# Kernel optimization log

Hardware: AMD Instinct MI355X
Metric: run time of the kernel (lower is better)

Reference implementation:

```python
import jax, jax.numpy as jnp
import numpy as np

EMB = 1024
HID = 4096
NHEADS = 16
DK = EMB // NHEADS
EPS = 1e-6
B, S = 2, 2048


def setup_inputs() -> dict:
    key = jax.random.key(0)
    ks = jax.random.split(key, 10)
    sc = 0.02
    return {
        "x": jax.random.normal(ks[0], (B, S, EMB), dtype=jnp.float32),
        "src_mask": jnp.ones((B, 1, 1, S), dtype=jnp.int32),
        "wq": jax.random.normal(ks[1], (EMB, EMB), dtype=jnp.float32) * sc,
        "wk": jax.random.normal(ks[2], (EMB, EMB), dtype=jnp.float32) * sc,
        "wv": jax.random.normal(ks[3], (EMB, EMB), dtype=jnp.float32) * sc,
        "wo": jax.random.normal(ks[4], (EMB, EMB), dtype=jnp.float32) * sc,
        "ff1_w": jax.random.normal(ks[5], (EMB, HID), dtype=jnp.float32) * sc,
        "ff1_b": jnp.zeros((HID,), dtype=jnp.float32),
        "ff2_w": jax.random.normal(ks[6], (HID, EMB), dtype=jnp.float32) * sc,
        "ff2_b": jnp.zeros((EMB,), dtype=jnp.float32),
        "ln1_a": jnp.ones((1,), dtype=jnp.float32),
        "ln1_b": jnp.zeros((1,), dtype=jnp.float32),
        "ln2_a": jnp.ones((1,), dtype=jnp.float32),
        "ln2_b": jnp.zeros((1,), dtype=jnp.float32),
    }


def layernorm(x, alpha, bias):
    # Faithful to the custom LayerNorm: scalar alpha/bias, std with Bessel
    # correction (torch default unbiased=True), divide by (std + eps).
    mean = jnp.mean(x, axis=-1, keepdims=True)
    var = jnp.sum((x - mean) ** 2, axis=-1, keepdims=True) / (x.shape[-1] - 1)
    std = jnp.sqrt(var)
    return alpha * (x - mean) / (std + EPS) + bias


def mha(x, mask, wq, wk, wv, wo):
    b, s, _ = x.shape
    def split_heads(t):  # [B,S,E] -> [B,H,S,dk]
        return t.reshape(b, s, NHEADS, DK).transpose(0, 2, 1, 3)
    q = split_heads(x @ wq)
    k = split_heads(x @ wk)
    v = split_heads(x @ wv)
    scores = jnp.einsum("bhqd,bhkd->bhqk", q, k) / jnp.sqrt(jnp.float32(DK))
    scores = jnp.where(mask == 0, -jnp.inf, scores)
    attn = jax.nn.softmax(scores, axis=-1)
    out = jnp.einsum("bhqk,bhkd->bhqd", attn, v)
    out = out.transpose(0, 2, 1, 3).reshape(b, s, EMB)
    return out @ wo


def ffn(x, w1, b1, w2, b2):
    return jax.nn.relu(x @ w1 + b1) @ w2 + b2


def reference(x, src_mask, wq, wk, wv, wo, ff1_w, ff1_b, ff2_w, ff2_b,
              ln1_a, ln1_b, ln2_a, ln2_b):
    # pre-norm residual encoder block (dropout=0 / eval mode)
    h = x + mha(layernorm(x, ln1_a, ln1_b), src_mask, wq, wk, wv, wo)
    out = h + ffn(layernorm(h, ln2_a, ln2_b), ff1_w, ff1_b, ff2_w, ff2_b)
    return out
```

## Files before the change

kernel.cpp:

```cpp
#include <hip/hip_runtime.h>
#include <stdint.h>

#define EMB 1024
#define HID 4096
#define NHEADS 16
#define DKH 64
#define SEQ 2048
#define BATCH 2
#define MROWS (BATCH * SEQ)
#define GBK 64

typedef unsigned short u16;
typedef unsigned int u32;
typedef __attribute__((ext_vector_type(8))) short short8;
typedef __attribute__((ext_vector_type(4))) float f32x4;
typedef __attribute__((ext_vector_type(16))) float f32x16;
typedef __attribute__((ext_vector_type(4))) u32 u32x4;
typedef __attribute__((ext_vector_type(2))) int i32x2;

#if __has_builtin(__builtin_amdgcn_exp2f)
#define QK_SCALE 0.18033688011f
#define QK_CLAMP 43.3f
__device__ __forceinline__ float pexp(float x) { return __builtin_amdgcn_exp2f(x); }
#else
#define QK_SCALE 0.125f
#define QK_CLAMP 30.0f
__device__ __forceinline__ float pexp(float x) { return __expf(x); }
#endif

__device__ __forceinline__ u16 f2bf(float f) {
    unsigned u = __float_as_uint(f);
    unsigned r = 0x7FFFu + ((u >> 16) & 1u);
    return (u16)((u + r) >> 16);
}
__device__ __forceinline__ f32x4 mfma16(short8 a, short8 b, f32x4 c) {
    return __builtin_amdgcn_mfma_f32_16x16x32_bf16(a, b, c, 0, 0, 0);
}
__device__ __forceinline__ f32x16 mfma32(short8 a, short8 b, f32x16 c) {
    return __builtin_amdgcn_mfma_f32_32x32x16_bf16(a, b, c, 0, 0, 0);
}
__device__ __forceinline__ void gl_lds16(const u16* g, u16* l) {
    __builtin_amdgcn_global_load_lds(
        (__attribute__((address_space(1))) void*)g,
        (__attribute__((address_space(3))) void*)l, 16, 0, 0);
}
__device__ __forceinline__ void plswap(u32& a, u32& b) {
#if __has_builtin(__builtin_amdgcn_permlane32_swap)
    i32x2 r = __builtin_amdgcn_permlane32_swap((int)a, (int)b, false, false);
    a = (u32)r.x; b = (u32)r.y;
#else
    const u32 ta = (u32)__shfl_xor((int)a, 32);
    const u32 tb = (u32)__shfl_xor((int)b, 32);
    const bool hi = (threadIdx.x & 32) != 0;
    const u32 na = hi ? tb : a;
    const u32 nb = hi ? b : ta;
    a = na; b = nb;
#endif
}
__device__ __forceinline__ short8 mk8(u32 a, u32 b, u32 c, u32 d) {
    u32x4 t; t.x = a; t.y = b; t.z = c; t.w = d;
    return __builtin_bit_cast(short8, t);
}

__global__ __launch_bounds__(256) void transpose_qkvo(
    const float* __restrict__ wq, const float* __restrict__ wk,
    const float* __restrict__ wv, const float* __restrict__ wo,
    u16* __restrict__ qkvT, u16* __restrict__ woT,
    const int* __restrict__ msk, int* __restrict__ flag) {
    __shared__ u16 t[32][33];
    const int z = blockIdx.z;
    const float* W = (z == 0) ? wq : (z == 1) ? wk : (z == 2) ? wv : wo;
    u16* WT = (z < 3) ? (qkvT + (size_t)z * EMB * EMB) : woT;
    const float scale = (z == 0) ? QK_SCALE : 1.0f;
    const int tx = threadIdx.x & 31, ty = threadIdx.x >> 5;
    const int k0 = blockIdx.y * 32, n0 = blockIdx.x * 32;
#pragma unroll
    for (int r = 0; r < 32; r += 8)
        t[ty + r][tx] = f2bf(scale * W[(size_t)(k0 + ty + r) * EMB + n0 + tx]);
    __syncthreads();
#pragma unroll
    for (int r = 0; r < 32; r += 8)
        WT[(size_t)(n0 + ty + r) * EMB + k0 + tx] = t[tx][ty + r];

    if (z == 3 && blockIdx.x == 0 && blockIdx.y == 0) {
        int v = 1;
        for (int i = threadIdx.x; i < BATCH * SEQ; i += 256)
            v &= (msk[i] != 0) ? 1 : 0;
        v = __all(v) ? 1 : 0;
        __shared__ int rr[4];
        if ((threadIdx.x & 63) == 0) rr[threadIdx.x >> 6] = v;
        __syncthreads();
        if (threadIdx.x == 0) flag[0] = rr[0] & rr[1] & rr[2] & rr[3];
    }
}

__global__ __launch_bounds__(256) void transpose_bf16(
    const float* __restrict__ W, u16* __restrict__ WT, int K, int N) {
    __shared__ u16 t[32][33];
    const int tx = threadIdx.x & 31, ty = threadIdx.x >> 5;
    const int k0 = blockIdx.y * 32, n0 = blockIdx.x * 32;
#pragma unroll
    for (int r = 0; r < 32; r += 8)
        t[ty + r][tx] = f2bf(W[(size_t)(k0 + ty + r) * N + n0 + tx]);
    __syncthreads();
#pragma unroll
    for (int r = 0; r < 32; r += 8)
        WT[(size_t)(n0 + ty + r) * K + k0 + tx] = t[tx][ty + r];
}

__global__ __launch_bounds__(256) void ln_kernel(
    const float* __restrict__ x, u16* __restrict__ out,
    const float* __restrict__ alpha_p, const float* __restrict__ beta_p) {
    const int row = blockIdx.x;
    const int tid = threadIdx.x;
    float4 v = reinterpret_cast<const float4*>(x + (size_t)row * EMB)[tid];

    __shared__ float red[4];
    float s = v.x + v.y + v.z + v.w;
    for (int off = 32; off; off >>= 1) s += __shfl_down(s, off);
    if ((tid & 63) == 0) red[tid >> 6] = s;
    __syncthreads();
    float mean = (red[0] + red[1] + red[2] + red[3]) * (1.0f / EMB);
    __syncthreads();

    float d0 = v.x - mean, d1 = v.y - mean, d2 = v.z - mean, d3 = v.w - mean;
    float sq = d0 * d0 + d1 * d1 + d2 * d2 + d3 * d3;
    for (int off = 32; off; off >>= 1) sq += __shfl_down(sq, off);
    if ((tid & 63) == 0) red[tid >> 6] = sq;
    __syncthreads();
    float var = (red[0] + red[1] + red[2] + red[3]) * (1.0f / (EMB - 1));
    float inv = 1.0f / (sqrtf(var) + 1e-6f);
    float a = alpha_p[0], b = beta_p[0];

    ushort4 o;
    o.x = f2bf(a * d0 * inv + b);
    o.y = f2bf(a * d1 * inv + b);
    o.z = f2bf(a * d2 * inv + b);
    o.w = f2bf(a * d3 * inv + b);
    reinterpret_cast<ushort4*>(out + (size_t)row * EMB)[tid] = o;
}

template <int BN, int NWM>
__global__ __launch_bounds__(512) void gemm_mfma(
    const u16* __restrict__ A, const u16* __restrict__ BT, void* C,
    const float* __restrict__ bias, const void* res,
    int M, int N, int K, int relu, int out_mode,
    u16* __restrict__ Kb_out, u16* __restrict__ VT_out) {
    constexpr int NWN = 8 / NWM;
    constexpr int WM = 128 / (16 * NWM);
    constexpr int WN = BN / (16 * NWN);
    constexpr int NBUF = (BN == 64) ? 3 : 2;
    __shared__ u16 As[NBUF][128][GBK];
    __shared__ u16 Bs[NBUF][BN][GBK];

    const int tid = threadIdx.x;
    const int wave = tid >> 6, lane = tid & 63;
    const int quad = lane >> 4, lc = lane & 15;
    const int wm = wave % NWM, wn = wave / NWM;

    const int nx = gridDim.x;
    const int bid = blockIdx.y * nx + blockIdx.x;
    const int xcd = bid & 7, sl = bid >> 3;
    const int nyx = gridDim.y >> 3;
    const int bcol = sl % nx;
    const int brow = (sl / nx) + xcd * nyx;
    const int row0 = brow * 128, col0 = bcol * BN;

    const int srow = lane >> 3;
    const int scg = (lane & 7) ^ srow;

    f32x4 acc[WM][WN] = {};

    auto stage = [&](int k0, int buf) {
#pragma unroll
        for (int i = 0; i < 2; ++i) {
            const int rb = wave * 16 + i * 8;
            gl_lds16(A + (size_t)(row0 + rb + srow) * K + k0 + scg * 8,
                     &As[buf][rb][0]);
        }
        if constexpr (BN == 128) {
#pragma unroll
            for (int i = 0; i < 2; ++i) {
                const int rb = wave * 16 + i * 8;
                gl_lds16(BT + (size_t)(col0 + rb + srow) * K + k0 + scg * 8,
                         &Bs[buf][rb][0]);
            }
        } else {
            const int rb = wave * 8;
            gl_lds16(BT + (size_t)(col0 + rb + srow) * K + k0 + scg * 8,
                     &Bs[buf][rb][0]);
        }
    };

    auto compute = [&](int cur) {
#pragma unroll
        for (int s = 0; s < 2; ++s) {
            short8 af[WM], bfv[WN];
#pragma unroll
            for (int i = 0; i < WM; ++i) {
                const int ar = wm * (16 * WM) + i * 16 + lc;
                af[i] = *reinterpret_cast<const short8*>(
                    &As[cur][ar][(((s * 4 + quad) ^ (ar & 7))) * 8]);
            }
#pragma unroll
            for (int j = 0; j < WN; ++j) {
                const int br = wn * (16 * WN) + j * 16 + lc;
                bfv[j] = *reinterpret_cast<const short8*>(
                    &Bs[cur][br][(((s * 4 + quad) ^ (br & 7))) * 8]);
            }
#pragma unroll
            for (int i = 0; i < WM; ++i)
#pragma unroll
                for (int j = 0; j < WN; ++j)
                    acc[i][j] = mfma16(af[i], bfv[j], acc[i][j]);
        }
    };

    if constexpr (NBUF == 2) {
        stage(0, 0);
        __syncthreads();
        int cur = 0;
        for (int k0 = 0; k0 < K; k0 += GBK) {
            if (k0 + GBK < K) stage(k0 + GBK, cur ^ 1);
            compute(cur);
            __syncthreads();
            cur ^= 1;
        }
    } else {
        stage(0, 0);
        if (GBK < K) stage(GBK, 1);
        int cur = 0;
        for (int k0 = 0; k0 < K; k0 += GBK) {
            if (k0 + 2 * GBK < K) {
                int nb = cur + 2; if (nb >= 3) nb -= 3;
                stage(k0 + 2 * GBK, nb);
            }
            const int rem = (K - k0) >> 6;
            if (rem > 2)       asm volatile("s_waitcnt vmcnt(6)" ::: "memory");
            else if (rem == 2) asm volatile("s_waitcnt vmcnt(3)" ::: "memory");
            else               asm volatile("s_waitcnt vmcnt(0)" ::: "memory");
            __builtin_amdgcn_s_barrier();
            __builtin_amdgcn_sched_barrier(0);
            compute(cur);
            __builtin_amdgcn_s_barrier();
            cur = (cur == 2) ? 0 : cur + 1;
        }
    }

    u16* Cb = (u16*)C;
    int mode = out_mode, ncols = N, lcol0 = col0;
    if (out_mode == 3) {
        const int seg = col0 >> 10;
        lcol0 = col0 & 1023;
        ncols = EMB;
        if (seg == 1) { Cb = Kb_out; mode = 0; }
        else if (seg == 2) { Cb = VT_out; mode = 2; }
        else { mode = 0; }
    }

#pragma unroll
    for (int j = 0; j < WN; ++j) {
        const int col = lcol0 + wn * (16 * WN) + j * 16 + lc;
        const float bv = bias ? bias[col] : 0.f;
#pragma unroll
        for (int i = 0; i < WM; ++i) {
            const int rbase = row0 + wm * (16 * WM) + i * 16 + quad * 4;
            if (mode == 2) {
                ushort4 o;
                o.x = f2bf(acc[i][j][0]); o.y = f2bf(acc[i][j][1]);
                o.z = f2bf(acc[i][j][2]); o.w = f2bf(acc[i][j][3]);
                *reinterpret_cast<ushort4*>(Cb + (size_t)col * M + rbase) = o;
            } else {
#pragma unroll
                for (int r = 0; r < 4; ++r) {
                    const size_t idx = (size_t)(rbase + r) * ncols + col;
                    float v = acc[i][j][r] + bv;
                    if (relu) v = fmaxf(v, 0.f);
                    if (res) v += ((const float*)res)[idx];
                    if (mode == 1) ((float*)C)[idx] = v;
                    else Cb[idx] = f2bf(v);
                }
            }
        }
    }
}

__global__ __launch_bounds__(512) void gemm_ws(
    const u16* __restrict__ A, const u16* __restrict__ BT, void* C,
    const float* __restrict__ bias, const void* res,
    int M, int N, int K, int relu, int fp32out) {
    __shared__ __align__(16) char smem[65536];
    u16 (*As)[128][GBK] = (u16(*)[128][GBK])smem;
    u16 (*Bs)[128][GBK] = (u16(*)[128][GBK])(smem + 32768);

    const int tid = threadIdx.x;
    const int wave = tid >> 6, lane = tid & 63;
    const int quad = lane >> 4, lc = lane & 15;
    const int p = wave >> 1, s = wave & 1;
    const int pm = p >> 1, pn = p & 1;

    const int nx = gridDim.x;
    const int bid = blockIdx.y * nx + blockIdx.x;
    const int xcd = bid & 7, sl = bid >> 3;
    const int nyx = gridDim.y >> 3;
    const int bcol = sl % nx;
    const int brow = (sl / nx) + xcd * nyx;
    const int row0 = brow * 128, col0 = bcol * 128;

    const int srow = lane >> 3;
    const int scg = (lane & 7) ^ srow;

    f32x4 acc[4][4] = {};

    auto stage = [&](int k0, int buf) {
#pragma unroll
        for (int i = 0; i < 2; ++i) {
            const int rb = wave * 16 + i * 8;
            gl_lds16(A + (size_t)(row0 + rb + srow) * K + k0 + scg * 8,
                     &As[buf][rb][0]);
        }
#pragma unroll
        for (int i = 0; i < 2; ++i) {
            const int rb = wave * 16 + i * 8;
            gl_lds16(BT + (size_t)(col0 + rb + srow) * K + k0 + scg * 8,
                     &Bs[buf][rb][0]);
        }
    };

    const int nt = K >> 6;
    stage(0, 0);
    int cur = 0;
    for (int t = 0; t < nt; ++t) {
        if (t + 1 < nt) {
            stage((t + 1) << 6, cur ^ 1);
            asm volatile("s_waitcnt vmcnt(4)" ::: "memory");
        } else {
            asm volatile("s_waitcnt vmcnt(0)" ::: "memory");
        }
        __builtin_amdgcn_s_barrier();
        __builtin_amdgcn_sched_barrier(0);

        short8 af[4], bfv[4];
#pragma unroll
        for (int i = 0; i < 4; ++i) {
            const int ar = pm * 64 + i * 16 + lc;
            af[i] = *reinterpret_cast<const short8*>(
                &As[cur][ar][(((s * 4 + quad) ^ (ar & 7))) * 8]);
        }
#pragma unroll
        for (int j = 0; j < 4; ++j) {
            const int br = pn * 64 + j * 16 + lc;
            bfv[j] = *reinterpret_cast<const short8*>(
                &Bs[cur][br][(((s * 4 + quad) ^ (br & 7))) * 8]);
        }
#pragma unroll
        for (int i = 0; i < 4; ++i)
#pragma unroll
            for (int j = 0; j < 4; ++j)
                acc[i][j] = mfma16(af[i], bfv[j], acc[i][j]);

        __builtin_amdgcn_s_barrier();
        cur ^= 1;
    }

    float* Ms = (float*)smem;
    if (s == 0) {
#pragma unroll
        for (int i = 0; i < 4; ++i)
#pragma unroll
            for (int j = 0; j < 4; ++j)
#pragma unroll
                for (int r = 0; r < 4; ++r)
                    Ms[(pm * 64 + i * 16 + quad * 4 + r) * 128 +
                       pn * 64 + j * 16 + lc] = acc[i][j][r];
    }
    __syncthreads();
    if (s == 1) {
#pragma unroll
        for (int i = 0; i < 4; ++i)
#pragma unroll
            for (int j = 0; j < 4; ++j)
#pragma unroll
                for (int r = 0; r < 4; ++r)
                    Ms[(pm * 64 + i * 16 + quad * 4 + r) * 128 +
                       pn * 64 + j * 16 + lc] += acc[i][j][r];
    }
    __syncthreads();

#pragma unroll
    for (int k = 0; k < 8; ++k) {
        const int fi = (k * 512 + tid) * 4;
        const int row = fi >> 7, col = fi & 127;
        const float4 v = *reinterpret_cast<const float4*>(&Ms[fi]);
        float o0 = v.x, o1 = v.y, o2 = v.z, o3 = v.w;
        if (bias) {
            const float4 bv = *reinterpret_cast<const float4*>(&bias[col0 + col]);
            o0 += bv.x; o1 += bv.y; o2 += bv.z; o3 += bv.w;
        }
        if (relu) {
            o0 = fmaxf(o0, 0.f); o1 = fmaxf(o1, 0.f);
            o2 = fmaxf(o2, 0.f); o3 = fmaxf(o3, 0.f);
        }
        const size_t gidx = (size_t)(row0 + row) * N + col0 + col;
        if (res) {
            const float4 rv = *reinterpret_cast<const float4*>(
                &((const float*)res)[gidx]);
            o0 += rv.x; o1 += rv.y; o2 += rv.z; o3 += rv.w;
        }
        if (fp32out) {
            float4 ov; ov.x = o0; ov.y = o1; ov.z = o2; ov.w = o3;
            *reinterpret_cast<float4*>(&((float*)C)[gidx]) = ov;
        } else {
            ushort4 ov;
            ov.x = f2bf(o0); ov.y = f2bf(o1); ov.z = f2bf(o2); ov.w = f2bf(o3);
            *reinterpret_cast<ushort4*>(&((u16*)C)[gidx]) = ov;
        }
    }
}

__global__ __launch_bounds__(512, 2) void attn_mfma(
    const u16* __restrict__ Q, const u16* __restrict__ K,
    const u16* __restrict__ VT, const int* __restrict__ mask,
    const int* __restrict__ mflag, u16* __restrict__ O) {
    const int tid = threadIdx.x;
    const int wave = tid >> 6, lane = tid & 63;
    const int hi = lane >> 5, ln31 = lane & 31;
    const int qp = wave >> 1, s = wave & 1;
    const int H = blockIdx.x & 31;
    const int qblk = blockIdx.x >> 5;
    const int h = H & 15, b = H >> 4;

    __shared__ __align__(16) char smem[70656];
    u16 (*Ks)[128][DKH] = (u16(*)[128][DKH])smem;
    u16 (*Vs)[DKH][128] = (u16(*)[DKH][128])(smem + 32768);

    const int fast = mflag[0];

    short8 qb[2][4];
#pragma unroll
    for (int t = 0; t < 2; ++t) {
        const u16* qsrc = Q + (size_t)(b * SEQ + qblk * 256 + qp * 64 + t * 32 + ln31) * EMB
                            + h * DKH + hi * 8;
#pragma unroll
        for (int f = 0; f < 4; ++f)
            qb[t][f] = *reinterpret_cast<const short8*>(qsrc + f * 16);
    }

    const int srow = lane >> 3, scg = (lane & 7) ^ srow;
    const int svr = lane >> 4, ssl = lane & 15;

    auto stage = [&](int kc, int buf) {
#pragma unroll
        for (int i = 0; i < 2; ++i) {
            const int t8 = wave * 16 + i * 8;
            gl_lds16(K + (size_t)(b * SEQ + kc + t8 + srow) * EMB + h * DKH + scg * 8,
                     &Ks[buf][t8][0]);
        }
#pragma unroll
        for (int i = 0; i < 2; ++i) {
            const int d4 = wave * 8 + i * 4;
            const int dim = d4 + svr;
            const int gv = ssl ^ (dim & 15);
            gl_lds16(VT + (size_t)(h * DKH + dim) * MROWS + b * SEQ + kc + gv * 8,
                     &Vs[buf][d4][0]);
        }
    };

    f32x16 o00 = {}, o01 = {}, o10 = {}, o11 = {};
    float rs0 = 0.f, rs1 = 0.f;
    const int tok0 = s * 64;

    const int NCH = SEQ / 128;
    stage(0, 0);
    int cur = 0;

    for (int tch = 0; tch < NCH; ++tch) {
        if (tch + 1 < NCH) {
            stage((tch + 1) * 128, cur ^ 1);
            asm volatile("s_waitcnt vmcnt(4)" ::: "memory");
        } else {
            asm volatile("s_waitcnt vmcnt(0)" ::: "memory");
        }
        __builtin_amdgcn_s_barrier();
        __builtin_amdgcn_sched_barrier(0);
        const int kc = tch * 128;

#pragma unroll
        for (int mt = 0; mt < 2; ++mt) {
            const int trow = tok0 + mt * 32 + ln31;
            f32x16 st0 = {}, st1 = {};
#pragma unroll
            for (int f = 0; f < 4; ++f) {
                const int slot = (2 * f + hi) ^ (trow & 7);
                const short8 ka = *reinterpret_cast<const short8*>(
                    &Ks[cur][trow][slot * 8]);
                st0 = mfma32(ka, qb[0][f], st0);
                st1 = mfma32(ka, qb[1][f], st1);
            }
            int4 mks[4];
            if (!fast) {
#pragma unroll
                for (int g = 0; g < 4; ++g)
                    mks[g] = *reinterpret_cast<const int4*>(
                        mask + b * SEQ + kc + tok0 + mt * 32 + g * 8 + hi * 4);
            }
            short8 fr[2][2];
#pragma unroll
            for (int t = 0; t < 2; ++t) {
                f32x16& st = t ? st1 : st0;
                if (fast) {
#pragma unroll
                    for (int r = 0; r < 16; ++r)
                        st[r] = pexp(fminf(st[r], QK_CLAMP));
                } else {
#pragma unroll
                    for (int g = 0; g < 4; ++g) {
                        const int* mkp = &mks[g].x;
#pragma unroll
                        for (int r4 = 0; r4 < 4; ++r4) {
                            const int r = g * 4 + r4;
                            const float pv = pexp(fminf(st[r], QK_CLAMP));
                            st[r] = mkp[r4] ? pv : 0.f;
                        }
                    }
                }
                const float sum =
                    (((st[0] + st[1]) + (st[2] + st[3])) +
                     ((st[4] + st[5]) + (st[6] + st[7]))) +
                    (((st[8] + st[9]) + (st[10] + st[11])) +
                     ((st[12] + st[13]) + (st[14] + st[15])));
                if (t) rs1 += sum; else rs0 += sum;

                u32 pk0 = __builtin_amdgcn_perm(__float_as_uint(st[1]),
                                                __float_as_uint(st[0]), 0x07060302u);
                u32 pk1 = __builtin_amdgcn_perm(__float_as_uint(st[3]),
                                                __float_as_uint(st[2]), 0x07060302u);
                u32 pk2 = __builtin_amdgcn_perm(__float_as_uint(st[5]),
                                                __float_as_uint(st[4]), 0x07060302u);
                u32 pk3 = __builtin_amdgcn_perm(__float_as_uint(st[7]),
                                                __float_as_uint(st[6]), 0x07060302u);
                u32 pk4 = __builtin_amdgcn_perm(__float_as_uint(st[9]),
                                                __float_as_uint(st[8]), 0x07060302u);
                u32 pk5 = __builtin_amdgcn_perm(__float_as_uint(st[11]),
                                                __float_as_uint(st[10]), 0x07060302u);
                u32 pk6 = __builtin_amdgcn_perm(__float_as_uint(st[13]),
                                                __float_as_uint(st[12]), 0x07060302u);
                u32 pk7 = __builtin_amdgcn_perm(__float_as_uint(st[15]),
                                                __float_as_uint(st[14]), 0x07060302u);
                plswap(pk0, pk2);
                plswap(pk1, pk3);
                plswap(pk4, pk6);
                plswap(pk5, pk7);
                fr[t][0] = mk8(pk0, pk1, pk2, pk3);
                fr[t][1] = mk8(pk4, pk5, pk6, pk7);
            }

#pragma unroll
            for (int sub = 0; sub < 2; ++sub) {
                const int g = s * 8 + (2 * mt + sub) * 2 + hi;
#pragma unroll
                for (int nt = 0; nt < 2; ++nt) {
                    const int drow = nt * 32 + ln31;
                    const short8 vb = *reinterpret_cast<const short8*>(
                        &Vs[cur][drow][(g ^ (drow & 15)) * 8]);
                    if (nt == 0) {
                        o00 = mfma32(fr[0][sub], vb, o00);
                        o10 = mfma32(fr[1][sub], vb, o10);
                    } else {
                        o01 = mfma32(fr[0][sub], vb, o01);
                        o11 = mfma32(fr[1][sub], vb, o11);
                    }
                }
            }
        }
        __builtin_amdgcn_s_barrier();
        cur ^= 1;
    }

    rs0 += __shfl_xor(rs0, 32);
    rs1 += __shfl_xor(rs1, 32);

    float* Om = (float*)smem;
    float* Ls = (float*)(smem + 69632);

    if (s == 0) {
#pragma unroll
        for (int t = 0; t < 2; ++t) {
            const int tile = qp * 2 + t;
#pragma unroll
            for (int nt = 0; nt < 2; ++nt) {
                const f32x16& ov = t ? (nt ? o11 : o10) : (nt ? o01 : o00);
#pragma unroll
                for (int r = 0; r < 16; ++r) {
                    const int row = (r & 3) + 8 * (r >> 2) + 4 * hi;
                    Om[(tile * 32 + row) * 68 + nt * 32 + ln31] = ov[r];
                }
            }
            if (lane < 32) Ls[tile * 32 + ln31] = t ? rs1 : rs0;
        }
    }
    __syncthreads();
    if (s == 1) {
#pragma unroll
        for (int t = 0; t < 2; ++t) {
            const int tile = qp * 2 + t;
            if (lane < 32) Ls[tile * 32 + ln31] += (t ? rs1 : rs0);
#pragma unroll
            for (int nt = 0; nt < 2; ++nt) {
                const f32x16& ov = t ? (nt ? o11 : o10) : (nt ? o01 : o00);
#pragma unroll
                for (int r = 0; r < 16; ++r) {
                    const int row = (r & 3) + 8 * (r >> 2) + 4 * hi;
                    Om[(tile * 32 + row) * 68 + nt * 32 + ln31] += ov[r];
                }
            }
        }
    }
    __syncthreads();

    {
        const int q = tid >> 1, seg = tid & 1;
        const float inv = 1.0f / Ls[q];
        const float* src = Om + q * 68 + seg * 32;
        u16* dst = O + (size_t)(b * SEQ + qblk * 256 + q) * EMB + h * DKH + seg * 32;
#pragma unroll
        for (int i = 0; i < 8; ++i) {
            const float4 v = *reinterpret_cast<const float4*>(src + i * 4);
            ushort4 ou;
            ou.x = f2bf(v.x * inv); ou.y = f2bf(v.y * inv);
            ou.z = f2bf(v.z * inv); ou.w = f2bf(v.w * inv);
            *reinterpret_cast<ushort4*>(dst + i * 4) = ou;
        }
    }
}

extern "C" void kernel_launch(void* const* d_in, const int* in_sizes, int n_in,
                              void* d_out, int out_size, void* d_ws, size_t ws_size,
                              hipStream_t stream) {
    const float* x     = (const float*)d_in[0];
    const int*   mask  = (const int*)d_in[1];
    const float* wq    = (const float*)d_in[2];
    const float* wk    = (const float*)d_in[3];
    const float* wv    = (const float*)d_in[4];
    const float* wo    = (const float*)d_in[5];
    const float* ff1_w = (const float*)d_in[6];
    const float* ff1_b = (const float*)d_in[7];
    const float* ff2_w = (const float*)d_in[8];
    const float* ff2_b = (const float*)d_in[9];
    const float* ln1_a = (const float*)d_in[10];
    const float* ln1_b = (const float*)d_in[11];
    const float* ln2_a = (const float*)d_in[12];
    const float* ln2_b = (const float*)d_in[13];
    float* out = (float*)d_out;

    char* ws = (char*)d_ws;
    const size_t MB = 1u << 20;
    u16* act   = (u16*)(ws + 0);
    u16* Qb    = (u16*)(ws + 8 * MB);
    u16* Kb    = (u16*)(ws + 16 * MB);
    u16* VTb   = (u16*)(ws + 24 * MB);
    int* mflag = (int*)(ws + 32 * MB);
    u16* f1    = (u16*)(ws + 8 * MB);
    u16* wqkvT = (u16*)(ws + 40 * MB);
    u16* woT   = (u16*)(ws + 46 * MB);
    u16* ffT   = (u16*)(ws + 40 * MB);

    transpose_qkvo<<<dim3(EMB / 32, EMB / 32, 4), 256, 0, stream>>>(
        wq, wk, wv, wo, wqkvT, woT, mask, mflag);

    ln_kernel<<<MROWS, 256, 0, stream>>>(x, act, ln1_a, ln1_b);

    gemm_mfma<128, 2><<<dim3(3 * EMB / 128, MROWS / 128), 512, 0, stream>>>(
        act, wqkvT, Qb, nullptr, nullptr, MROWS, 3 * EMB, EMB, 0, 3, Kb, VTb);

    attn_mfma<<<BATCH * NHEADS * (SEQ / 256), 512, 0, stream>>>(
        Qb, Kb, VTb, mask, mflag, act);

    gemm_mfma<64, 4><<<dim3(EMB / 64, MROWS / 128), 512, 0, stream>>>(
        act, woT, out, nullptr, x, MROWS, EMB, EMB, 0, 1, nullptr, nullptr);

    ln_kernel<<<MROWS, 256, 0, stream>>>(out, act, ln2_a, ln2_b);

    transpose_bf16<<<dim3(HID / 32, EMB / 32), 256, 0, stream>>>(ff1_w, ffT, EMB, HID);
    gemm_ws<<<dim3(HID / 128, MROWS / 128), 512, 0, stream>>>(
        act, ffT, f1, ff1_b, nullptr, MROWS, HID, EMB, 1, 0);

    transpose_bf16<<<dim3(EMB / 32, HID / 32), 256, 0, stream>>>(ff2_w, ffT, HID, EMB);
    gemm_ws<<<dim3(EMB / 128, MROWS / 128), 512, 0, stream>>>(
        f1, ffT, out, ff2_b, out, MROWS, EMB, HID, 0, 1);
}
```

Baseline: 338.7 us.

## Split attention keys across four waves per query pair, halve query block

Each attention block now covers 128 queries instead of 256, and the eight waves form two query pairs, each with four waves splitting every 128-key chunk into 32-key slices. This doubles the grid so more blocks fill the GPU. Partial outputs and row sums from the four key slices are reduced in two shared-memory buffers and combined at write-out. In exchange, K/V staging into LDS is repeated for twice as many blocks, and the final reduction does more work per query.

```diff
diff --git a/kernel.cpp b/kernel.cpp
--- a/kernel.cpp
+++ b/kernel.cpp
@@ -425,7 +425,7 @@
     const int tid = threadIdx.x;
     const int wave = tid >> 6, lane = tid & 63;
     const int hi = lane >> 5, ln31 = lane & 31;
-    const int qp = wave >> 1, s = wave & 1;
+    const int qp = wave >> 2, s = wave & 3;
     const int H = blockIdx.x & 31;
     const int qblk = blockIdx.x >> 5;
     const int h = H & 15, b = H >> 4;
@@ -439,7 +439,7 @@
     short8 qb[2][4];
 #pragma unroll
     for (int t = 0; t < 2; ++t) {
-        const u16* qsrc = Q + (size_t)(b * SEQ + qblk * 256 + qp * 64 + t * 32 + ln31) * EMB
+        const u16* qsrc = Q + (size_t)(b * SEQ + qblk * 128 + qp * 64 + t * 32 + ln31) * EMB
                             + h * DKH + hi * 8;
 #pragma unroll
         for (int f = 0; f < 4; ++f)
@@ -468,7 +468,7 @@
 
     f32x16 o00 = {}, o01 = {}, o10 = {}, o11 = {};
     float rs0 = 0.f, rs1 = 0.f;
-    const int tok0 = s * 64;
+    const int tok0 = s * 32;
 
     const int NCH = SEQ / 128;
     stage(0, 0);
@@ -485,91 +485,88 @@
         __builtin_amdgcn_sched_barrier(0);
         const int kc = tch * 128;
 
-#pragma unroll
-        for (int mt = 0; mt < 2; ++mt) {
-            const int trow = tok0 + mt * 32 + ln31;
-            f32x16 st0 = {}, st1 = {};
-#pragma unroll
-            for (int f = 0; f < 4; ++f) {
-                const int slot = (2 * f + hi) ^ (trow & 7);
-                const short8 ka = *reinterpret_cast<const short8*>(
-                    &Ks[cur][trow][slot * 8]);
-                st0 = mfma32(ka, qb[0][f], st0);
-                st1 = mfma32(ka, qb[1][f], st1);
-            }
-            int4 mks[4];
-            if (!fast) {
-#pragma unroll
-                for (int g = 0; g < 4; ++g)
-                    mks[g] = *reinterpret_cast<const int4*>(
-                        mask + b * SEQ + kc + tok0 + mt * 32 + g * 8 + hi * 4);
-            }
-            short8 fr[2][2];
-#pragma unroll
-            for (int t = 0; t < 2; ++t) {
-                f32x16& st = t ? st1 : st0;
-                if (fast) {
-#pragma unroll
-                    for (int r = 0; r < 16; ++r)
-                        st[r] = pexp(fminf(st[r], QK_CLAMP));
-                } else {
-#pragma unroll
-                    for (int g = 0; g < 4; ++g) {
-                        const int* mkp = &mks[g].x;
-#pragma unroll
-                        for (int r4 = 0; r4 < 4; ++r4) {
-                            const int r = g * 4 + r4;
-                            const float pv = pexp(fminf(st[r], QK_CLAMP));
-                            st[r] = mkp[r4] ? pv : 0.f;
-                        }
+        const int trow = tok0 + ln31;
+        f32x16 st0 = {}, st1 = {};
+#pragma unroll
+        for (int f = 0; f < 4; ++f) {
+            const int slot = (2 * f + hi) ^ (trow & 7);
+            const short8 ka = *reinterpret_cast<const short8*>(
+                &Ks[cur][trow][slot * 8]);
+            st0 = mfma32(ka, qb[0][f], st0);
+            st1 = mfma32(ka, qb[1][f], st1);
+        }
+        int4 mks[4];
+        if (!fast) {
+#pragma unroll
+            for (int g = 0; g < 4; ++g)
+                mks[g] = *reinterpret_cast<const int4*>(
+                    mask + b * SEQ + kc + tok0 + g * 8 + hi * 4);
+        }
+        short8 fr[2][2];
+#pragma unroll
+        for (int t = 0; t < 2; ++t) {
+            f32x16& st = t ? st1 : st0;
+            if (fast) {
+#pragma unroll
+                for (int r = 0; r < 16; ++r)
+                    st[r] = pexp(fminf(st[r], QK_CLAMP));
+            } else {
+#pragma unroll
+                for (int g = 0; g < 4; ++g) {
+                    const int* mkp = &mks[g].x;
+#pragma unroll
+                    for (int r4 = 0; r4 < 4; ++r4) {
+                        const int r = g * 4 + r4;
+                        const float pv = pexp(fminf(st[r], QK_CLAMP));
+                        st[r] = mkp[r4] ? pv : 0.f;
                     }
                 }
-                const float sum =
-                    (((st[0] + st[1]) + (st[2] + st[3])) +
-                     ((st[4] + st[5]) + (st[6] + st[7]))) +
-                    (((st[8] + st[9]) + (st[10] + st[11])) +
-                     ((st[12] + st[13]) + (st[14] + st[15])));
-                if (t) rs1 += sum; else rs0 += sum;
-
-                u32 pk0 = __builtin_amdgcn_perm(__float_as_uint(st[1]),
-                                                __float_as_uint(st[0]), 0x07060302u);
-                u32 pk1 = __builtin_amdgcn_perm(__float_as_uint(st[3]),
-                                                __float_as_uint(st[2]), 0x07060302u);
-                u32 pk2 = __builtin_amdgcn_perm(__float_as_uint(st[5]),
-                                                __float_as_uint(st[4]), 0x07060302u);
-                u32 pk3 = __builtin_amdgcn_perm(__float_as_uint(st[7]),
-                                                __float_as_uint(st[6]), 0x07060302u);
-                u32 pk4 = __builtin_amdgcn_perm(__float_as_uint(st[9]),
-                                                __float_as_uint(st[8]), 0x07060302u);
-                u32 pk5 = __builtin_amdgcn_perm(__float_as_uint(st[11]),
-                                                __float_as_uint(st[10]), 0x07060302u);
-                u32 pk6 = __builtin_amdgcn_perm(__float_as_uint(st[13]),
-                                                __float_as_uint(st[12]), 0x07060302u);
-                u32 pk7 = __builtin_amdgcn_perm(__float_as_uint(st[15]),
-                                                __float_as_uint(st[14]), 0x07060302u);
-                plswap(pk0, pk2);
-                plswap(pk1, pk3);
-                plswap(pk4, pk6);
-                plswap(pk5, pk7);
-                fr[t][0] = mk8(pk0, pk1, pk2, pk3);
-                fr[t][1] = mk8(pk4, pk5, pk6, pk7);
-            }
-
-#pragma unroll
-            for (int sub = 0; sub < 2; ++sub) {
-                const int g = s * 8 + (2 * mt + sub) * 2 + hi;
-#pragma unroll
-                for (int nt = 0; nt < 2; ++nt) {
-                    const int drow = nt * 32 + ln31;
-                    const short8 vb = *reinterpret_cast<const short8*>(
-                        &Vs[cur][drow][(g ^ (drow & 15)) * 8]);
-                    if (nt == 0) {
-                        o00 = mfma32(fr[0][sub], vb, o00);
-                        o10 = mfma32(fr[1][sub], vb, o10);
-                    } else {
-                        o01 = mfma32(fr[0][sub], vb, o01);
-                        o11 = mfma32(fr[1][sub], vb, o11);
-                    }
+            }
+            const float sum =
+                (((st[0] + st[1]) + (st[2] + st[3])) +
+                 ((st[4] + st[5]) + (st[6] + st[7]))) +
+                (((st[8] + st[9]) + (st[10] + st[11])) +
+                 ((st[12] + st[13]) + (st[14] + st[15])));
+            if (t) rs1 += sum; else rs0 += sum;
+
+            u32 pk0 = __builtin_amdgcn_perm(__float_as_uint(st[1]),
+                                            __float_as_uint(st[0]), 0x07060302u);
+            u32 pk1 = __builtin_amdgcn_perm(__float_as_uint(st[3]),
+                                            __float_as_uint(st[2]), 0x07060302u);
+            u32 pk2 = __builtin_amdgcn_perm(__float_as_uint(st[5]),
+                                            __float_as_uint(st[4]), 0x07060302u);
+            u32 pk3 = __builtin_amdgcn_perm(__float_as_uint(st[7]),
+                                            __float_as_uint(st[6]), 0x07060302u);
+            u32 pk4 = __builtin_amdgcn_perm(__float_as_uint(st[9]),
+                                            __float_as_uint(st[8]), 0x07060302u);
+            u32 pk5 = __builtin_amdgcn_perm(__float_as_uint(st[11]),
+                                            __float_as_uint(st[10]), 0x07060302u);
+            u32 pk6 = __builtin_amdgcn_perm(__float_as_uint(st[13]),
+                                            __float_as_uint(st[12]), 0x07060302u);
+            u32 pk7 = __builtin_amdgcn_perm(__float_as_uint(st[15]),
+                                            __float_as_uint(st[14]), 0x07060302u);
+            plswap(pk0, pk2);
+            plswap(pk1, pk3);
+            plswap(pk4, pk6);
+            plswap(pk5, pk7);
+            fr[t][0] = mk8(pk0, pk1, pk2, pk3);
+            fr[t][1] = mk8(pk4, pk5, pk6, pk7);
+        }
+
+#pragma unroll
+        for (int sub = 0; sub < 2; ++sub) {
+            const int g = s * 4 + sub * 2 + hi;
+#pragma unroll
+            for (int nt = 0; nt < 2; ++nt) {
+                const int drow = nt * 32 + ln31;
+                const short8 vb = *reinterpret_cast<const short8*>(
+                    &Vs[cur][drow][(g ^ (drow & 15)) * 8]);
+                if (nt == 0) {
+                    o00 = mfma32(fr[0][sub], vb, o00);
+                    o10 = mfma32(fr[1][sub], vb, o10);
+                } else {
+                    o01 = mfma32(fr[0][sub], vb, o01);
+                    o11 = mfma32(fr[1][sub], vb, o11);
                 }
             }
         }
@@ -580,10 +577,14 @@
     rs0 += __shfl_xor(rs0, 32);
     rs1 += __shfl_xor(rs1, 32);
 
-    float* Om = (float*)smem;
-    float* Ls = (float*)(smem + 69632);
-
-    if (s == 0) {
+    float* OmA = (float*)smem;
+    float* OmB = (float*)(smem + 34816);
+    float* LsA = (float*)(smem + 69632);
+    float* LsB = (float*)(smem + 70144);
+    float* Om = (s < 2) ? OmA : OmB;
+    float* Ls = (s < 2) ? LsA : LsB;
+
+    if ((s & 1) == 0) {
 #pragma unroll
         for (int t = 0; t < 2; ++t) {
             const int tile = qp * 2 + t;
@@ -600,7 +601,7 @@
         }
     }
     __syncthreads();
-    if (s == 1) {
+    if ((s & 1) == 1) {
 #pragma unroll
         for (int t = 0; t < 2; ++t) {
             const int tile = qp * 2 + t;
@@ -619,16 +620,18 @@
     __syncthreads();
 
     {
-        const int q = tid >> 1, seg = tid & 1;
-        const float inv = 1.0f / Ls[q];
-        const float* src = Om + q * 68 + seg * 32;
-        u16* dst = O + (size_t)(b * SEQ + qblk * 256 + q) * EMB + h * DKH + seg * 32;
-#pragma unroll
-        for (int i = 0; i < 8; ++i) {
-            const float4 v = *reinterpret_cast<const float4*>(src + i * 4);
+        const int q = tid >> 2, seg = tid & 3;
+        const float inv = 1.0f / (LsA[q] + LsB[q]);
+        const float* srcA = OmA + q * 68 + seg * 16;
+        const float* srcB = OmB + q * 68 + seg * 16;
+        u16* dst = O + (size_t)(b * SEQ + qblk * 128 + q) * EMB + h * DKH + seg * 16;
+#pragma unroll
+        for (int i = 0; i < 4; ++i) {
+            const float4 va = *reinterpret_cast<const float4*>(srcA + i * 4);
+            const float4 vb = *reinterpret_cast<const float4*>(srcB + i * 4);
             ushort4 ou;
-            ou.x = f2bf(v.x * inv); ou.y = f2bf(v.y * inv);
-            ou.z = f2bf(v.z * inv); ou.w = f2bf(v.w * inv);
+            ou.x = f2bf((va.x + vb.x) * inv); ou.y = f2bf((va.y + vb.y) * inv);
+            ou.z = f2bf((va.z + vb.z) * inv); ou.w = f2bf((va.w + vb.w) * inv);
             *reinterpret_cast<ushort4*>(dst + i * 4) = ou;
         }
     }
@@ -673,7 +676,7 @@
     gemm_mfma<128, 2><<<dim3(3 * EMB / 128, MROWS / 128), 512, 0, stream>>>(
         act, wqkvT, Qb, nullptr, nullptr, MROWS, 3 * EMB, EMB, 0, 3, Kb, VTb);
 
-    attn_mfma<<<BATCH * NHEADS * (SEQ / 256), 512, 0, stream>>>(
+    attn_mfma<<<BATCH * NHEADS * (SEQ / 128), 512, 0, stream>>>(
         Qb, Kb, VTb, mask, mflag, act);
 
     gemm_mfma<64, 4><<<dim3(EMB / 64, MROWS / 128), 512, 0, stream>>>(
```

Measured after the change: 364.7 us. 7.7% more time.
